# Kernel optimization log

Measured on AMD Instinct MI355X. Metric: run time of the kernel, lower is better.

## Reference

```python
import jax, jax.numpy as jnp
import numpy as np

HS = 1024          # hidden_size
NH_ATTN = 16       # attention heads
NH_LACT = 4        # lact fast-weight heads
DIN = HS // NH_LACT  # 256
DH = DIN             # inter_multi = 1
CHUNK = 1024       # lact_chunk_size
EPS = 1e-5


def setup_inputs() -> dict:
    key = jax.random.key(0)
    ks = jax.random.split(key, 6)
    B, S = 1, 4096
    x = jax.random.normal(ks[0], (B, S, HS), jnp.float32)
    ln_w = jnp.ones((HS,), jnp.float32)
    ln_b = jnp.zeros((HS,), jnp.float32)
    in_proj_w = jax.random.normal(ks[1], (3 * HS, HS), jnp.float32) * (HS ** -0.5)
    in_proj_b = jnp.zeros((3 * HS,), jnp.float32)
    out_proj_w = jax.random.normal(ks[2], (HS, HS), jnp.float32) * (HS ** -0.5)
    out_proj_b = jnp.zeros((HS,), jnp.float32)
    w0 = jax.random.normal(ks[3], (NH_LACT, DH, DIN), jnp.float32) / np.sqrt(DIN)
    w1 = jax.random.normal(ks[4], (NH_LACT, DIN, DH), jnp.float32) / np.sqrt(DH)
    w2 = jax.random.normal(ks[5], (NH_LACT, DH, DIN), jnp.float32) / np.sqrt(DIN)
    return dict(x=x, ln_w=ln_w, ln_b=ln_b, in_proj_w=in_proj_w, in_proj_b=in_proj_b,
                out_proj_w=out_proj_w, out_proj_b=out_proj_b, w0=w0, w1=w1, w2=w2)


def reference(x, ln_w, ln_b, in_proj_w, in_proj_b, out_proj_w, out_proj_b, w0, w1, w2):
    B, S, D = x.shape
    # LayerNorm
    mu = jnp.mean(x, axis=-1, keepdims=True)
    var = jnp.var(x, axis=-1, keepdims=True)
    xn = (x - mu) * jax.lax.rsqrt(var + EPS) * ln_w + ln_b

    # --- torch nn.MultiheadAttention(batch_first=True), self-attention, no mask ---
    qkv = xn @ in_proj_w.T + in_proj_b                      # [B,S,3D]
    q, k, v = jnp.split(qkv, 3, axis=-1)
    hd = D // NH_ATTN
    def heads(t):
        return t.reshape(B, S, NH_ATTN, hd).transpose(0, 2, 1, 3)  # [B,H,S,hd]
    q = heads(q) * (hd ** -0.5)
    k = heads(k)
    v = heads(v)
    attn = jax.nn.softmax(jnp.einsum('bhqd,bhkd->bhqk', q, k), axis=-1)
    ao = jnp.einsum('bhqk,bhkd->bhqd', attn, v).transpose(0, 2, 1, 3).reshape(B, S, D)
    attn_out = ao @ out_proj_w.T + out_proj_b

    # --- chunked fast-weight SwiGLU TTT (block_causal_lact_swiglu) ---
    # q=k=v=chunk; lr0=lr1=lr2=1; each outer chunk is one TTT step starting from
    # the module parameters: update weights on (k,v) then apply to q (block-causal).
    nc = S // CHUNK
    c = xn.reshape(B, nc, CHUNK, NH_LACT, DIN).transpose(0, 1, 3, 2, 4)  # [B,nc,nh,C,din]
    kv = c  # k == v == q == chunk

    # fast-weight SwiGLU forward on keys: f(k) = w1 @ (silu(w0 k) * (w2 k))
    gate = jnp.einsum('bnhcd,hed->bnhce', kv, w0)     # [B,nc,nh,C,dh]
    sg = jax.nn.sigmoid(gate)
    h = gate * sg                                     # silu
    g = jnp.einsum('bnhcd,hed->bnhce', kv, w2)
    hidden = h * g

    # negative dot-product loss L = -sum(v * f(k)) -> dOut = -v
    dout = -kv                                        # [B,nc,nh,C,din]
    dhid = jnp.einsum('bnhcd,hde->bnhce', dout, w1)
    dh = dhid * g
    dg = dhid * h
    dpre = dh * (sg + gate * sg * (1.0 - sg))         # silu'
    dw1 = jnp.einsum('bnhcd,bnhce->bnhde', dout, hidden)
    dw0 = jnp.einsum('bnhce,bnhcd->bnhed', dpre, kv)
    dw2 = jnp.einsum('bnhce,bnhcd->bnhed', dg, kv)

    # SGD step (lr = 1)
    w0n = w0 - dw0   # [B,nc,nh,dh,din]
    w1n = w1 - dw1
    w2n = w2 - dw2

    # apply updated fast weights to queries
    gq = jnp.einsum('bnhcd,bnhed->bnhce', c, w0n)
    hq = gq * jax.nn.sigmoid(gq)
    gq2 = jnp.einsum('bnhcd,bnhed->bnhce', c, w2n)
    oq = jnp.einsum('bnhce,bnhde->bnhcd', hq * gq2, w1n)  # [B,nc,nh,C,din]
    lact_out = oq.transpose(0, 1, 3, 2, 4).reshape(B, S, D)

    return lact_out + attn_out
```

## Files before the change

kernel.cpp:

```cpp
#include <hip/hip_runtime.h>
#include <hip/hip_bf16.h>


typedef __bf16 bf16_t;
typedef __bf16 bf16x8 __attribute__((ext_vector_type(8)));
typedef __bf16 bf16x4 __attribute__((ext_vector_type(4)));
typedef float  f32x4  __attribute__((ext_vector_type(4)));
typedef float  f32x16 __attribute__((ext_vector_type(16)));

#define SW64(r,cg) ((cg) ^ ((r)&7))
#define SW32(r,cg) ((cg) ^ (((r)>>2)&3))

static __device__ __forceinline__ f32x4 mfma16(bf16x8 a, bf16x8 b, f32x4 c){
  return __builtin_amdgcn_mfma_f32_16x16x32_bf16(a, b, c, 0, 0, 0);
}
static __device__ __forceinline__ f32x16 mfma32(bf16x8 a, bf16x8 b, f32x16 c){
  return __builtin_amdgcn_mfma_f32_32x32x16_bf16(a, b, c, 0, 0, 0);
}
__device__ __forceinline__ float sigm(float x){ return 1.0f/(1.0f + __expf(-x)); }
static __device__ __forceinline__ unsigned pkbf(float lo, float hi){
  unsigned short a = __builtin_bit_cast(unsigned short, (__bf16)lo);
  unsigned short b = __builtin_bit_cast(unsigned short, (__bf16)hi);
  return (unsigned)a | ((unsigned)b<<16);
}
static __device__ __forceinline__ float unpk_lo(unsigned u){
  return (float)__builtin_bit_cast(__bf16,(unsigned short)(u&0xffffu));
}
static __device__ __forceinline__ float unpk_hi(unsigned u){
  return (float)__builtin_bit_cast(__bf16,(unsigned short)(u>>16));
}
static __device__ __forceinline__ float hswap_add(float x){
  float a=x, b=x;
  asm volatile("v_permlane32_swap_b32 %0, %1" : "+v"(a), "+v"(b));
  return a+b;
}

__global__ __launch_bounds__(256) void ln_kernel(const float* __restrict__ x,
    const float* __restrict__ w, const float* __restrict__ b,
    bf16_t* __restrict__ xnb)
{
  int s = blockIdx.x, t = threadIdx.x;
  const float4* xr = (const float4*)(x + (size_t)s*1024);
  float4 v = xr[t];
  float sum = v.x+v.y+v.z+v.w;
  float ss  = v.x*v.x+v.y*v.y+v.z*v.z+v.w*v.w;
  #pragma unroll
  for (int o=32;o>0;o>>=1){ sum += __shfl_down(sum,o); ss += __shfl_down(ss,o); }
  __shared__ float red[8];
  __shared__ float stats[2];
  int wid=t>>6, lane=t&63;
  if(lane==0){ red[wid]=sum; red[4+wid]=ss; }
  __syncthreads();
  if(t==0){
    float S0=red[0]+red[1]+red[2]+red[3];
    float Q0=red[4]+red[5]+red[6]+red[7];
    float mu=S0*(1.0f/1024.0f);
    float var=Q0*(1.0f/1024.0f)-mu*mu;
    stats[0]=mu; stats[1]=rsqrtf(var+1e-5f);
  }
  __syncthreads();
  float mu=stats[0], rs=stats[1];
  float4 wv=((const float4*)w)[t], bv=((const float4*)b)[t];
  float4 o;
  o.x=(v.x-mu)*rs*wv.x+bv.x;
  o.y=(v.y-mu)*rs*wv.y+bv.y;
  o.z=(v.z-mu)*rs*wv.z+bv.z;
  o.w=(v.w-mu)*rs*wv.w+bv.w;
  bf16x4 ob = { (bf16_t)o.x, (bf16_t)o.y, (bf16_t)o.z, (bf16_t)o.w };
  *(bf16x4*)&xnb[(size_t)s*1024 + t*4] = ob;
}

__global__ __launch_bounds__(256) void prep_weights(
  const float* __restrict__ ipw, const float* __restrict__ opw,
  const float* __restrict__ w0, const float* __restrict__ w2,
  const float* __restrict__ w1,
  bf16_t* __restrict__ ipwb, bf16_t* __restrict__ opwb,
  bf16_t* __restrict__ w0b, bf16_t* __restrict__ w2b, bf16_t* __restrict__ w1tb)
{
  long i = ((long)blockIdx.x*256 + threadIdx.x)*4;
  if (i < 3145728) {
    float4 v = *(const float4*)(ipw + i);
    bf16x4 o = {(bf16_t)v.x,(bf16_t)v.y,(bf16_t)v.z,(bf16_t)v.w};
    *(bf16x4*)&ipwb[i] = o;
  } else if (i < 4194304) {
    long j = i - 3145728;
    float4 v = *(const float4*)(opw + j);
    bf16x4 o = {(bf16_t)v.x,(bf16_t)v.y,(bf16_t)v.z,(bf16_t)v.w};
    *(bf16x4*)&opwb[j] = o;
  } else if (i < 4456448) {
    long j = i - 4194304;
    float4 v = *(const float4*)(w0 + j);
    bf16x4 o = {(bf16_t)v.x,(bf16_t)v.y,(bf16_t)v.z,(bf16_t)v.w};
    *(bf16x4*)&w0b[j] = o;
  } else if (i < 4718592) {
    long j = i - 4456448;
    float4 v = *(const float4*)(w2 + j);
    bf16x4 o = {(bf16_t)v.x,(bf16_t)v.y,(bf16_t)v.z,(bf16_t)v.w};
    *(bf16x4*)&w2b[j] = o;
  } else if (i < 4980736) {
    long j = i - 4718592;
    int h = (int)(j>>16), rem = (int)(j&65535), d = rem>>8, e0 = rem&255;
    float4 v = *(const float4*)(w1 + j);
    bf16_t* dst = w1tb + h*65536 + d;
    dst[(e0+0)*256] = (bf16_t)v.x;
    dst[(e0+1)*256] = (bf16_t)v.y;
    dst[(e0+2)*256] = (bf16_t)v.z;
    dst[(e0+3)*256] = (bf16_t)v.w;
  }
}

__global__ __launch_bounds__(256) void xnT_kernel(const bf16_t* __restrict__ xnb,
                                                  bf16_t* __restrict__ xt)
{
  int dt = blockIdx.x, ct = blockIdx.y, bz = blockIdx.z;
  int nb = bz>>2, hb = bz&3;
  int t = threadIdx.x;
  __shared__ __align__(16) bf16_t T[4096];
  int r = t>>2, seg = t&3;
  const bf16_t* src = xnb + ((size_t)nb*1024 + ct*64 + r)*1024 + hb*256 + dt*64 + seg*16;
  uint4 a0 = *(const uint4*)src;
  uint4 a1 = *(const uint4*)(src + 8);
  *(uint4*)&T[r*64 + ((((seg*2  )&7)^(r&7))<<3)] = a0;
  *(uint4*)&T[r*64 + ((((seg*2+1)&7)^(r&7))<<3)] = a1;
  __syncthreads();
  int d = t>>2, s2 = t&3;
  unsigned uu[8];
  #pragma unroll
  for (int p=0;p<8;p++){
    int c0 = s2*16 + 2*p, c1 = c0+1;
    unsigned short e0 = __builtin_bit_cast(unsigned short,
        T[c0*64 + (((d>>3)^(c0&7))<<3) + (d&7)]);
    unsigned short e1 = __builtin_bit_cast(unsigned short,
        T[c1*64 + (((d>>3)^(c1&7))<<3) + (d&7)]);
    uu[p] = (unsigned)e0 | ((unsigned)e1<<16);
  }
  uint4 o0 = {uu[0],uu[1],uu[2],uu[3]}, o1 = {uu[4],uu[5],uu[6],uu[7]};
  bf16_t* dst = xt + (size_t)bz*262144 + (size_t)(dt*64 + d)*1024 + ct*64 + s2*16;
  *(uint4*)dst = o0;
  *(uint4*)(dst+8) = o1;
}

__device__ __forceinline__ void gemm_core(
    const bf16_t* __restrict__ A, int lda,
    const bf16_t* __restrict__ B, int ldb,
    int K, int m0, int n0, f32x4 (&acc)[4][4])
{
  int t = threadIdx.x, l = t&63;
  int w = t>>6, wr = w>>1, wc = w&1;
  __shared__ __align__(16) bf16_t As[4096], Bs[4096];
  int r0 = t>>2, c0 = t&3, r1 = r0+64;
  const bf16_t* Arow0 = A + (size_t)(m0+r0)*lda + c0*8;
  const bf16_t* Arow1 = A + (size_t)(m0+r1)*lda + c0*8;
  const bf16_t* Brow0 = B + (size_t)(n0+r0)*ldb + c0*8;
  const bf16_t* Brow1 = B + (size_t)(n0+r1)*ldb + c0*8;
  uint4 av0 = *(const uint4*)Arow0, av1 = *(const uint4*)Arow1;
  uint4 bv0 = *(const uint4*)Brow0, bv1 = *(const uint4*)Brow1;
  int wo0 = r0*32 + (SW32(r0,c0)<<3), wo1 = r1*32 + (SW32(r1,c0)<<3);

  for (int k0=0; k0<K; k0+=32) {
    if (k0) __syncthreads();
    *(uint4*)&As[wo0] = av0; *(uint4*)&As[wo1] = av1;
    *(uint4*)&Bs[wo0] = bv0; *(uint4*)&Bs[wo1] = bv1;
    __syncthreads();
    if (k0+32 < K) {
      av0 = *(const uint4*)(Arow0 + k0+32); av1 = *(const uint4*)(Arow1 + k0+32);
      bv0 = *(const uint4*)(Brow0 + k0+32); bv1 = *(const uint4*)(Brow1 + k0+32);
    }
    bf16x8 af[4], bb[4];
    #pragma unroll
    for (int mt=0;mt<4;mt++){
      int row = (wr<<6)+(mt<<4)+(l&15);
      af[mt] = *(bf16x8*)&As[row*32 + (SW32(row, (l>>4))<<3)];
    }
    #pragma unroll
    for (int nt=0;nt<4;nt++){
      int row = (wc<<6)+(nt<<4)+(l&15);
      bb[nt] = *(bf16x8*)&Bs[row*32 + (SW32(row, (l>>4))<<3)];
    }
    #pragma unroll
    for (int mt=0;mt<4;mt++)
      #pragma unroll
      for (int nt=0;nt<4;nt++)
        acc[mt][nt] = mfma16(af[mt], bb[nt], acc[mt][nt]);
  }
}

__device__ __forceinline__ void gemm_core_w(
    const bf16_t* __restrict__ A, int lda,
    const bf16_t* __restrict__ B, int ldb,
    int K, int m0, int n0, f32x4 (&acc)[4][2])
{
  int t = threadIdx.x, l = t&63;
  int w = t>>6, wr = w>>1, wc = w&1;
  __shared__ __align__(16) bf16_t As[4096], Bs[2048];
  int r0 = t>>2, c0 = t&3, r1 = r0+64;
  const bf16_t* Arow0 = A + (size_t)(m0+r0)*lda + c0*8;
  const bf16_t* Arow1 = A + (size_t)(m0+r1)*lda + c0*8;
  const bf16_t* Brow  = B + (size_t)(n0+r0)*ldb + c0*8;
  uint4 av0 = *(const uint4*)Arow0, av1 = *(const uint4*)Arow1;
  uint4 bv  = *(const uint4*)Brow;
  int wo0 = r0*32 + (SW32(r0,c0)<<3), wo1 = r1*32 + (SW32(r1,c0)<<3);

  for (int k0=0; k0<K; k0+=32) {
    if (k0) __syncthreads();
    *(uint4*)&As[wo0] = av0; *(uint4*)&As[wo1] = av1;
    *(uint4*)&Bs[wo0] = bv;
    __syncthreads();
    if (k0+32 < K) {
      av0 = *(const uint4*)(Arow0 + k0+32); av1 = *(const uint4*)(Arow1 + k0+32);
      bv  = *(const uint4*)(Brow + k0+32);
    }
    bf16x8 af[4], bb[2];
    #pragma unroll
    for (int mt=0;mt<4;mt++){
      int row = (wr<<6)+(mt<<4)+(l&15);
      af[mt] = *(bf16x8*)&As[row*32 + (SW32(row, (l>>4))<<3)];
    }
    #pragma unroll
    for (int nt=0;nt<2;nt++){
      int row = (wc<<5)+(nt<<4)+(l&15);
      bb[nt] = *(bf16x8*)&Bs[row*32 + (SW32(row, (l>>4))<<3)];
    }
    #pragma unroll
    for (int mt=0;mt<4;mt++)
      #pragma unroll
      for (int nt=0;nt<2;nt++)
        acc[mt][nt] = mfma16(af[mt], bb[nt], acc[mt][nt]);
  }
}

#define EPILOOP(...) { int l=threadIdx.x&63, w_=threadIdx.x>>6, wr=w_>>1, wc=w_&1; \
  _Pragma("unroll") for(int mt=0;mt<4;mt++) _Pragma("unroll") for(int nt=0;nt<4;nt++) \
  _Pragma("unroll") for(int q=0;q<4;q++){ \
    int gr=m0+(wr<<6)+(mt<<4)+((l>>4)<<2)+q; int gc=n0+(wc<<6)+(nt<<4)+(l&15); \
    float v=acc[mt][nt][q]; __VA_ARGS__ } }

#define ACCZERO(acc) \
  _Pragma("unroll") for(int i_=0;i_<4;i_++) _Pragma("unroll") for(int j_=0;j_<4;j_++){ \
    f32x4 z_={0.f,0.f,0.f,0.f}; acc[i_][j_]=z_; }

#define ACCZERO_W(acc) \
  _Pragma("unroll") for(int i_=0;i_<4;i_++) _Pragma("unroll") for(int j_=0;j_<2;j_++){ \
    f32x4 z_={0.f,0.f,0.f,0.f}; acc[i_][j_]=z_; }

template<int EPI>
__global__ __launch_bounds__(256) void gemm_big(
  const bf16_t* __restrict__ A, const bf16_t* __restrict__ B,
  float* __restrict__ C, const float* __restrict__ bias,
  bf16_t* __restrict__ O1, bf16_t* __restrict__ O2, bf16_t* __restrict__ O3,
  int K, int ldc)
{
  int m0 = blockIdx.y<<7, n0 = blockIdx.x<<7;
  f32x4 acc[4][4];
  ACCZERO(acc)
  gemm_core(A, K, B, K, K, m0, n0, acc);
  EPILOOP(
    if constexpr (EPI==1) {
      C[(size_t)gr*ldc + gc] = v + bias[gc];
    } else {
      v += bias[gc];
      int seg = gc>>10; int c2 = gc&1023; int hh = c2>>6; int dd = c2&63;
      size_t oi = ((size_t)hh*4096 + gr)*64 + dd;
      if (seg==0)      O1[oi] = (bf16_t)(v*0.18033688011112042f);
      else if (seg==1) O2[oi] = (bf16_t)v;
      else             O3[oi] = (bf16_t)v;
    }
  )
}

__global__ __launch_bounds__(256) void lact_fwd_ew(
    const bf16_t* __restrict__ xnb,
    const bf16_t* __restrict__ w0b, const bf16_t* __restrict__ w2b,
    const bf16_t* __restrict__ w1tb,
    bf16_t* __restrict__ hT, bf16_t* __restrict__ pT, bf16_t* __restrict__ gT)
{
  int bz = blockIdx.z, hb = bz&3;
  const bf16_t* A = xnb + (size_t)(bz>>2)*1048576 + (size_t)hb*256;
  int m0 = blockIdx.y<<7, n0 = blockIdx.x<<6;
  f32x4 acc[4][2];
  unsigned gpk[4][2][2], ppk[4][2][2];

  ACCZERO_W(acc)
  gemm_core_w(A, 1024, w0b + hb*65536, 256, 256, m0, n0, acc);
  #pragma unroll
  for (int mt=0;mt<4;mt++)
    #pragma unroll
    for (int nt=0;nt<2;nt++){
      gpk[mt][nt][0] = pkbf(acc[mt][nt][0], acc[mt][nt][1]);
      gpk[mt][nt][1] = pkbf(acc[mt][nt][2], acc[mt][nt][3]);
    }
  __syncthreads();
  ACCZERO_W(acc)
  gemm_core_w(A, 1024, w2b + hb*65536, 256, 256, m0, n0, acc);
  #pragma unroll
  for (int mt=0;mt<4;mt++)
    #pragma unroll
    for (int nt=0;nt<2;nt++){
      ppk[mt][nt][0] = pkbf(acc[mt][nt][0], acc[mt][nt][1]);
      ppk[mt][nt][1] = pkbf(acc[mt][nt][2], acc[mt][nt][3]);
    }
  __syncthreads();
  ACCZERO_W(acc)
  gemm_core_w(A, 1024, w1tb + hb*65536, 256, 256, m0, n0, acc);

  int l=threadIdx.x&63, w_=threadIdx.x>>6, wr=w_>>1, wc=w_&1;
  size_t tb = (size_t)bz*262144;
  #pragma unroll
  for (int mt=0;mt<4;mt++){
    #pragma unroll
    for (int nt=0;nt<2;nt++){
      int gc = n0 + (wc<<5) + (nt<<4) + (l&15);
      size_t rowoff = tb + (size_t)gc*1024;
      #pragma unroll
      for (int qp=0;qp<2;qp++){
        int gr0 = m0 + (wr<<6) + (mt<<4) + ((l>>4)<<2) + 2*qp;
        float gate0 = unpk_lo(gpk[mt][nt][qp]), gate1 = unpk_hi(gpk[mt][nt][qp]);
        float g0 = unpk_lo(ppk[mt][nt][qp]), g1 = unpk_hi(ppk[mt][nt][qp]);
        float dh0 = acc[mt][nt][2*qp], dh1 = acc[mt][nt][2*qp+1];
        float sg0 = sigm(gate0), sg1 = sigm(gate1);
        float hs0 = gate0*sg0, hs1 = gate1*sg1;
        float hid0 = hs0*g0, hid1 = hs1*g1;
        float nd0 = -dh0, nd1 = -dh1;
        float dpre0 = nd0*g0*(sg0 + gate0*sg0*(1.0f-sg0));
        float dpre1 = nd1*g1*(sg1 + gate1*sg1*(1.0f-sg1));
        float dg0 = nd0*hs0, dg1 = nd1*hs1;
        *(unsigned*)&hT[rowoff + gr0] = pkbf(hid0, hid1);
        *(unsigned*)&pT[rowoff + gr0] = pkbf(dpre0, dpre1);
        *(unsigned*)&gT[rowoff + gr0] = pkbf(dg0, dg1);
      }
    }
  }
}

__global__ __launch_bounds__(256) void lact_apply_u(
    const bf16_t* __restrict__ xnb,
    const bf16_t* __restrict__ w0nb, const bf16_t* __restrict__ w2nb,
    bf16_t* __restrict__ u)
{
  int bz = blockIdx.z;
  const bf16_t* A = xnb + (size_t)(bz>>2)*1048576 + (size_t)(bz&3)*256;
  int m0 = blockIdx.y<<7, n0 = blockIdx.x<<6;
  f32x4 acc[4][2];
  unsigned qpk[4][2][2];

  ACCZERO_W(acc)
  gemm_core_w(A, 1024, w2nb + (size_t)bz*65536, 256, 256, m0, n0, acc);
  #pragma unroll
  for (int mt=0;mt<4;mt++)
    #pragma unroll
    for (int nt=0;nt<2;nt++){
      qpk[mt][nt][0] = pkbf(acc[mt][nt][0], acc[mt][nt][1]);
      qpk[mt][nt][1] = pkbf(acc[mt][nt][2], acc[mt][nt][3]);
    }
  __syncthreads();
  ACCZERO_W(acc)
  gemm_core_w(A, 1024, w0nb + (size_t)bz*65536, 256, 256, m0, n0, acc);

  int l=threadIdx.x&63, w_=threadIdx.x>>6, wr=w_>>1, wc=w_&1;
  size_t tb = (size_t)bz*262144;
  #pragma unroll
  for (int mt=0;mt<4;mt++){
    #pragma unroll
    for (int nt=0;nt<2;nt++){
      int gc = n0 + (wc<<5) + (nt<<4) + (l&15);
      #pragma unroll
      for (int qp=0;qp<2;qp++){
        int gr0 = m0 + (wr<<6) + (mt<<4) + ((l>>4)<<2) + 2*qp;
        float q20 = unpk_lo(qpk[mt][nt][qp]), q21 = unpk_hi(qpk[mt][nt][qp]);
        float gq0 = acc[mt][nt][2*qp], gq1 = acc[mt][nt][2*qp+1];
        u[tb + (size_t)gr0*256 + gc]     = (bf16_t)(gq0*sigm(gq0)*q20);
        u[tb + (size_t)(gr0+1)*256 + gc] = (bf16_t)(gq1*sigm(gq1)*q21);
      }
    }
  }
}

__global__ __launch_bounds__(256) void lact_upd(
    const bf16_t* __restrict__ xnTb, const bf16_t* __restrict__ hTb,
    const bf16_t* __restrict__ pTb,  const bf16_t* __restrict__ gTb,
    const float* __restrict__ w1, const float* __restrict__ w0,
    const float* __restrict__ w2,
    bf16_t* __restrict__ w1nb, bf16_t* __restrict__ w0nb, bf16_t* __restrict__ w2nb)
{
  int zz = blockIdx.z, sub = zz>>4, bz = zz&15, hb = bz&3;
  const bf16_t* A = (sub==0? xnTb : (sub==1? pTb : gTb)) + (size_t)bz*262144;
  const bf16_t* B = (sub==0? hTb : xnTb) + (size_t)bz*262144;
  const float*  P = (sub==0? w1 : (sub==1? w0 : w2)) + (size_t)hb*65536;
  bf16_t*       O = (sub==0? w1nb : (sub==1? w0nb : w2nb)) + (size_t)bz*65536;
  float sgn = (sub==0) ? 1.0f : -1.0f;
  int m0 = blockIdx.y<<7, n0 = blockIdx.x<<6;
  f32x4 acc[4][2];
  ACCZERO_W(acc)
  gemm_core_w(A, 1024, B, 1024, 1024, m0, n0, acc);
  int l=threadIdx.x&63, w_=threadIdx.x>>6, wr=w_>>1, wc=w_&1;
  #pragma unroll
  for (int mt=0;mt<4;mt++){
    #pragma unroll
    for (int nt=0;nt<2;nt++){
      int gc = n0 + (wc<<5) + (nt<<4) + (l&15);
      #pragma unroll
      for (int q=0;q<4;q++){
        int gr = m0 + (wr<<6) + (mt<<4) + ((l>>4)<<2) + q;
        O[(size_t)gr*256 + gc] =
            (bf16_t)(P[(size_t)gr*256 + gc] + sgn*acc[mt][nt][q]);
      }
    }
  }
}

__global__ __launch_bounds__(256) void lact_final(
    const bf16_t* __restrict__ u, const bf16_t* __restrict__ w1nb,
    float* __restrict__ out)
{
  int bz = blockIdx.z;
  const bf16_t* A = u + (size_t)bz*262144;
  const bf16_t* B = w1nb + (size_t)bz*65536;
  float* C = out + (size_t)(bz>>2)*1048576 + (size_t)(bz&3)*256;
  int m0 = blockIdx.y<<7, n0 = (blockIdx.x&1)<<7;
  f32x4 acc[4][4];
  ACCZERO(acc)
  gemm_core(A, 256, B, 256, 256, m0, n0, acc);
  EPILOOP( C[(size_t)gr*1024 + gc] += v; )
}

__global__ __launch_bounds__(256) void vtrans(const bf16_t* __restrict__ Vb,
                                              bf16_t* __restrict__ Vt)
{
  int st = blockIdx.x, h = blockIdx.y, t = threadIdx.x;
  __shared__ __align__(16) bf16_t T[64*72];
  #pragma unroll
  for (int G=t; G<512; G+=256) {
    int r = G>>3, cg = G&7;
    *(uint4*)&T[r*72 + cg*8] =
      *(const uint4*)(Vb + ((size_t)h*4096 + st*64 + r)*64 + cg*8);
  }
  __syncthreads();
  int d = t>>2, seg = t&3;
  bf16x8 e0, e1;
  #pragma unroll
  for (int i=0;i<8;i++)  e0[i] = T[(seg*16+i)*72 + d];
  #pragma unroll
  for (int i=0;i<8;i++)  e1[i] = T[(seg*16+8+i)*72 + d];
  size_t base = ((size_t)h*64 + d)*4096 + st*64 + seg*16;
  *(bf16x8*)(Vt + base)     = e0;
  *(bf16x8*)(Vt + base + 8) = e1;
}

__global__ __launch_bounds__(256) void attn_mfma3(
    const bf16_t* __restrict__ Qb, const bf16_t* __restrict__ Kb,
    const bf16_t* __restrict__ Vt, float* __restrict__ Opart,
    float* __restrict__ lpart)
{
  int h = blockIdx.x, qblk = blockIdx.y, z = blockIdx.z;
  int t = threadIdx.x, w = t>>6, l = t&63;
  int lh = l>>5, lq = l&31;
  __shared__ __align__(16) bf16_t Ks[4096], Vs[4096];

  const bf16_t* Kg = Kb + (size_t)h*262144 + (size_t)z*131072;
  const bf16_t* Vg = Vt + (size_t)h*262144 + (size_t)z*2048;

  bf16x8 qf[4];
  {
    const bf16_t* Qg = Qb + ((size_t)h*4096 + (size_t)qblk*128 + w*32 + lq)*64 + lh*8;
    #pragma unroll
    for (int s=0;s<4;s++) qf[s] = *(const bf16x8*)(Qg + s*16);
  }

  int r0 = t>>3, c0 = t&7, r1 = r0+32;
  uint4 kv0 = *(const uint4*)(Kg + (size_t)r0*64 + c0*8);
  uint4 kv1 = *(const uint4*)(Kg + (size_t)r1*64 + c0*8);
  uint4 vv0 = *(const uint4*)(Vg + (size_t)r0*4096 + c0*8);
  uint4 vv1 = *(const uint4*)(Vg + (size_t)r1*4096 + c0*8);

  float l_r = 0.f;
  f32x16 Oa, Ob;
  #pragma unroll
  for (int i=0;i<16;i++){ Oa[i]=0.f; Ob[i]=0.f; }

  int wo0 = r0*64 + (SW64(r0,c0)<<3);
  int wo1 = r1*64 + (SW64(r1,c0)<<3);

  for (int kt=0; kt<32; ++kt) {
    __syncthreads();
    *(uint4*)&Ks[wo0] = kv0;
    *(uint4*)&Ks[wo1] = kv1;
    *(uint4*)&Vs[wo0] = vv0;
    *(uint4*)&Vs[wo1] = vv1;
    __syncthreads();
    if (kt < 31) {
      const bf16_t* Kg2 = Kg + (size_t)(kt+1)*4096;
      kv0 = *(const uint4*)(Kg2 + (size_t)r0*64 + c0*8);
      kv1 = *(const uint4*)(Kg2 + (size_t)r1*64 + c0*8);
      const bf16_t* Vg2 = Vg + (kt+1)*64;
      vv0 = *(const uint4*)(Vg2 + (size_t)r0*4096 + c0*8);
      vv1 = *(const uint4*)(Vg2 + (size_t)r1*4096 + c0*8);
    }
    f32x16 S0, S1;
    #pragma unroll
    for (int i=0;i<16;i++){ S0[i]=0.f; S1[i]=0.f; }
    __builtin_amdgcn_s_setprio(1);
    #pragma unroll
    for (int s=0;s<4;s++){
      int g = (s<<1) + lh;
      bf16x8 k0 = *(const bf16x8*)&Ks[lq*64 + (SW64(lq,g)<<3)];
      int rowb = 32 + lq;
      bf16x8 k1 = *(const bf16x8*)&Ks[rowb*64 + (SW64(rowb,g)<<3)];
      S0 = mfma32(k0, qf[s], S0);
      S1 = mfma32(k1, qf[s], S1);
    }
    __builtin_amdgcn_s_setprio(0);
    #pragma unroll
    for (int i=0;i<16;i++) S0[i] = exp2f(S0[i]);
    #pragma unroll
    for (int i=0;i<16;i++) S1[i] = exp2f(S1[i]);
    float rt[8];
    #pragma unroll
    for (int i=0;i<8;i++) rt[i] = (S0[i]+S0[i+8]) + (S1[i]+S1[i+8]);
    #pragma unroll
    for (int i=0;i<4;i++) rt[i] += rt[i+4];
    l_r += (rt[0]+rt[1])+(rt[2]+rt[3]);
    unsigned pk0[4][2], pk1[4][2];
    #pragma unroll
    for (int u2=0; u2<4; u2++){
      #pragma unroll
      for (int wd=0; wd<2; wd++){
        int q0 = 4*u2 + 2*wd;
        pk0[u2][wd] = pkbf(S0[q0], S0[q0+1]);
        pk1[u2][wd] = pkbf(S1[q0], S1[q0+1]);
      }
    }
    __builtin_amdgcn_s_setprio(1);
    #pragma unroll
    for (int ks=0; ks<4; ks++){
      int v0 = 2*(ks&1);
      unsigned x0, x1, y0, y1;
      if (ks < 2) { x0 = pk0[v0][0]; x1 = pk0[v0][1]; y0 = pk0[v0+1][0]; y1 = pk0[v0+1][1]; }
      else        { x0 = pk1[v0][0]; x1 = pk1[v0][1]; y0 = pk1[v0+1][0]; y1 = pk1[v0+1][1]; }
      asm volatile("v_permlane32_swap_b32 %0, %1" : "+v"(x0), "+v"(y0));
      asm volatile("v_permlane32_swap_b32 %0, %1" : "+v"(x1), "+v"(y1));
      uint4 pau = {x0, x1, y0, y1};
      bf16x8 pa = __builtin_bit_cast(bf16x8, pau);
      int g = (ks<<1) + lh;
      bf16x8 vf0 = *(const bf16x8*)&Vs[lq*64 + (SW64(lq,g)<<3)];
      int rowb = 32 + lq;
      bf16x8 vf1 = *(const bf16x8*)&Vs[rowb*64 + (SW64(rowb,g)<<3)];
      Oa = mfma32(pa, vf0, Oa);
      Ob = mfma32(pa, vf1, Ob);
    }
    __builtin_amdgcn_s_setprio(0);
  }
  l_r = hswap_add(l_r);
  size_t pb = ((size_t)(h*32+qblk))*2 + z;
  float* Op = Opart + pb*8192 + (size_t)(w*32)*64;
  #pragma unroll
  for (int reg=0; reg<16; reg++){
    int row = (reg&3) + 8*(reg>>2) + 4*lh;
    Op[row*64 + lq]      = Oa[reg];
    Op[row*64 + 32 + lq] = Ob[reg];
  }
  if (l < 32) {
    lpart[pb*128 + (size_t)(w*32+l)] = l_r;
  }
}

__global__ __launch_bounds__(256) void attn_merge(
    const float* __restrict__ Opart, const float* __restrict__ lpart,
    bf16_t* __restrict__ ao)
{
  int h = blockIdx.x, qblk = blockIdx.y, t = threadIdx.x;
  int r = t>>1, ch = (t&1)<<5;
  size_t b = ((size_t)(h*32+qblk))*2;
  const float* O0 = Opart + b*8192;
  const float* O1 = O0 + 8192;
  float inv = 1.0f/(lpart[b*128 + r] + lpart[b*128 + 128 + r]);
  bf16_t* dst = ao + (size_t)(qblk*128+r)*1024 + h*64 + ch;
  const float* p0 = O0 + r*64 + ch;
  const float* p1 = O1 + r*64 + ch;
  #pragma unroll
  for (int j=0;j<8;j++){
    float4 o0 = *(const float4*)(p0 + j*4);
    float4 o1 = *(const float4*)(p1 + j*4);
    bf16x4 ov;
    ov[0]=(bf16_t)((o0.x+o1.x)*inv);
    ov[1]=(bf16_t)((o0.y+o1.y)*inv);
    ov[2]=(bf16_t)((o0.z+o1.z)*inv);
    ov[3]=(bf16_t)((o0.w+o1.w)*inv);
    *(bf16x4*)(dst + j*4) = ov;
  }
}

extern "C" void kernel_launch(void* const* d_in, const int* in_sizes, int n_in,
                              void* d_out, int out_size, void* d_ws, size_t ws_size,
                              hipStream_t stream) {
  const float* x          = (const float*)d_in[0];
  const float* ln_w       = (const float*)d_in[1];
  const float* ln_b       = (const float*)d_in[2];
  const float* in_proj_w  = (const float*)d_in[3];
  const float* in_proj_b  = (const float*)d_in[4];
  const float* out_proj_w = (const float*)d_in[5];
  const float* out_proj_b = (const float*)d_in[6];
  const float* w0         = (const float*)d_in[7];
  const float* w1         = (const float*)d_in[8];
  const float* w2         = (const float*)d_in[9];
  float* out = (float*)d_out;

  float* ws = (float*)d_ws;
  bf16_t* xnb  = (bf16_t*)(ws);
  bf16_t* Qb   = (bf16_t*)(ws + 2097152);
  bf16_t* Kb   = (bf16_t*)(ws + 4194304);
  bf16_t* Vb   = (bf16_t*)(ws + 6291456);
  bf16_t* ub   = (bf16_t*)(ws + 6291456);
  bf16_t* aob  = (bf16_t*)(ws + 10485760);
  bf16_t* Vtp  = (bf16_t*)(ws + 14680064);
  bf16_t* xnTb = (bf16_t*)(ws + 18874368);
  bf16_t* hTb  = (bf16_t*)(ws + 20971520);
  bf16_t* pTb  = (bf16_t*)(ws + 23068672);
  bf16_t* gTb  = (bf16_t*)(ws + 25165824);
  float*  Opart= ws + 18874368;
  bf16_t* ipwb = (bf16_t*)(ws + 27262976);
  float*  lp   = ws + 27262976;
  bf16_t* opwb = (bf16_t*)(ws + 28835840);
  bf16_t* w0b  = (bf16_t*)(ws + 29360128);
  bf16_t* w2b  = (bf16_t*)(ws + 29491200);
  bf16_t* w1tb = (bf16_t*)(ws + 29622272);
  bf16_t* w0nb = (bf16_t*)(ws + 29753344);
  bf16_t* w1nb = (bf16_t*)(ws + 30277632);
  bf16_t* w2nb = (bf16_t*)(ws + 30801920);

  dim3 blk(256);

  ln_kernel<<<dim3(4096),blk,0,stream>>>(x, ln_w, ln_b, xnb);

  prep_weights<<<dim3(4864),blk,0,stream>>>(in_proj_w, out_proj_w, w0, w2, w1,
                                            ipwb, opwb, w0b, w2b, w1tb);

  gemm_big<3><<<dim3(24,32),blk,0,stream>>>(
      xnb, ipwb, nullptr, in_proj_b, Qb, Kb, Vb, 1024, 0);

  vtrans<<<dim3(64,16),blk,0,stream>>>(Vb, Vtp);

  attn_mfma3<<<dim3(16,32,2),blk,0,stream>>>(Qb, Kb, Vtp, Opart, lp);

  attn_merge<<<dim3(16,32),blk,0,stream>>>(Opart, lp, aob);

  gemm_big<1><<<dim3(8,32),blk,0,stream>>>(
      aob, opwb, out, out_proj_b, nullptr,nullptr,nullptr, 1024, 1024);

  xnT_kernel<<<dim3(4,16,16),blk,0,stream>>>(xnb, xnTb);

  lact_fwd_ew<<<dim3(4,8,16),blk,0,stream>>>(xnb, w0b, w2b, w1tb, hTb, pTb, gTb);

  lact_upd<<<dim3(4,2,48),blk,0,stream>>>(xnTb, hTb, pTb, gTb,
                                          w1, w0, w2, w1nb, w0nb, w2nb);

  lact_apply_u<<<dim3(4,8,16),blk,0,stream>>>(xnb, w0nb, w2nb, ub);

  lact_final<<<dim3(2,8,16),blk,0,stream>>>(ub, w1nb, out);
}
```

Measured before the change: 385.6 us.

## Double-buffer GEMM and attention tiles via direct global-to-LDS async loads

Replaces the register-staged global loads plus LDS stores in the GEMM cores and the attention kernel with global_load_lds direct copies into double-buffered shared memory, prefetching the next K-tile while the current one is consumed. Swizzling moves to the global address side so LDS writes stay linear. The attention inner loop is also split into two 32-row halves to reduce live S registers. The cost is doubled LDS footprint, which may lower occupancy, and one barrier per iteration is kept.

Result: slower. 395.9 us (+2.7%).

```diff
diff --git a/kernel.cpp b/kernel.cpp
--- a/kernel.cpp
+++ b/kernel.cpp
@@ -33,6 +33,11 @@
   float a=x, b=x;
   asm volatile("v_permlane32_swap_b32 %0, %1" : "+v"(a), "+v"(b));
   return a+b;
+}
+static __device__ __forceinline__ void gload16(const bf16_t* g, bf16_t* l){
+  __builtin_amdgcn_global_load_lds(
+      (const __attribute__((address_space(1))) void*)g,
+      (__attribute__((address_space(3))) void*)l, 16, 0, 0);
 }
 
 __global__ __launch_bounds__(256) void ln_kernel(const float* __restrict__ x,
@@ -147,41 +152,45 @@
 {
   int t = threadIdx.x, l = t&63;
   int w = t>>6, wr = w>>1, wc = w&1;
-  __shared__ __align__(16) bf16_t As[4096], Bs[4096];
-  int r0 = t>>2, c0 = t&3, r1 = r0+64;
-  const bf16_t* Arow0 = A + (size_t)(m0+r0)*lda + c0*8;
-  const bf16_t* Arow1 = A + (size_t)(m0+r1)*lda + c0*8;
-  const bf16_t* Brow0 = B + (size_t)(n0+r0)*ldb + c0*8;
-  const bf16_t* Brow1 = B + (size_t)(n0+r1)*ldb + c0*8;
-  uint4 av0 = *(const uint4*)Arow0, av1 = *(const uint4*)Arow1;
-  uint4 bv0 = *(const uint4*)Brow0, bv1 = *(const uint4*)Brow1;
-  int wo0 = r0*32 + (SW32(r0,c0)<<3), wo1 = r1*32 + (SW32(r1,c0)<<3);
-
+  __shared__ __align__(16) bf16_t As[2][4096], Bs[2][4096];
+  int row0 = t>>2, gs0 = t&3;
+  int swz = (gs0 ^ ((row0>>2)&3))<<3;
+  const bf16_t* Aa = A + (size_t)(m0+row0)*lda + swz;
+  const bf16_t* Ba = B + (size_t)(n0+row0)*ldb + swz;
+  size_t lda64 = (size_t)64*lda, ldb64 = (size_t)64*ldb;
+
+  gload16(Aa,         &As[0][t*8]);
+  gload16(Aa + lda64, &As[0][(t+256)*8]);
+  gload16(Ba,         &Bs[0][t*8]);
+  gload16(Ba + ldb64, &Bs[0][(t+256)*8]);
+  __syncthreads();
+  int cur = 0;
   for (int k0=0; k0<K; k0+=32) {
-    if (k0) __syncthreads();
-    *(uint4*)&As[wo0] = av0; *(uint4*)&As[wo1] = av1;
-    *(uint4*)&Bs[wo0] = bv0; *(uint4*)&Bs[wo1] = bv1;
-    __syncthreads();
     if (k0+32 < K) {
-      av0 = *(const uint4*)(Arow0 + k0+32); av1 = *(const uint4*)(Arow1 + k0+32);
-      bv0 = *(const uint4*)(Brow0 + k0+32); bv1 = *(const uint4*)(Brow1 + k0+32);
+      int nb2 = cur^1;
+      gload16(Aa + k0+32,         &As[nb2][t*8]);
+      gload16(Aa + lda64 + k0+32, &As[nb2][(t+256)*8]);
+      gload16(Ba + k0+32,         &Bs[nb2][t*8]);
+      gload16(Ba + ldb64 + k0+32, &Bs[nb2][(t+256)*8]);
     }
     bf16x8 af[4], bb[4];
     #pragma unroll
     for (int mt=0;mt<4;mt++){
       int row = (wr<<6)+(mt<<4)+(l&15);
-      af[mt] = *(bf16x8*)&As[row*32 + (SW32(row, (l>>4))<<3)];
+      af[mt] = *(bf16x8*)&As[cur][row*32 + (SW32(row, (l>>4))<<3)];
     }
     #pragma unroll
     for (int nt=0;nt<4;nt++){
       int row = (wc<<6)+(nt<<4)+(l&15);
-      bb[nt] = *(bf16x8*)&Bs[row*32 + (SW32(row, (l>>4))<<3)];
+      bb[nt] = *(bf16x8*)&Bs[cur][row*32 + (SW32(row, (l>>4))<<3)];
     }
     #pragma unroll
     for (int mt=0;mt<4;mt++)
       #pragma unroll
       for (int nt=0;nt<4;nt++)
         acc[mt][nt] = mfma16(af[mt], bb[nt], acc[mt][nt]);
+    __syncthreads();
+    cur ^= 1;
   }
 }
 
@@ -192,40 +201,43 @@
 {
   int t = threadIdx.x, l = t&63;
   int w = t>>6, wr = w>>1, wc = w&1;
-  __shared__ __align__(16) bf16_t As[4096], Bs[2048];
-  int r0 = t>>2, c0 = t&3, r1 = r0+64;
-  const bf16_t* Arow0 = A + (size_t)(m0+r0)*lda + c0*8;
-  const bf16_t* Arow1 = A + (size_t)(m0+r1)*lda + c0*8;
-  const bf16_t* Brow  = B + (size_t)(n0+r0)*ldb + c0*8;
-  uint4 av0 = *(const uint4*)Arow0, av1 = *(const uint4*)Arow1;
-  uint4 bv  = *(const uint4*)Brow;
-  int wo0 = r0*32 + (SW32(r0,c0)<<3), wo1 = r1*32 + (SW32(r1,c0)<<3);
-
+  __shared__ __align__(16) bf16_t As[2][4096], Bs[2][2048];
+  int row0 = t>>2, gs0 = t&3;
+  int swz = (gs0 ^ ((row0>>2)&3))<<3;
+  const bf16_t* Aa = A + (size_t)(m0+row0)*lda + swz;
+  const bf16_t* Ba = B + (size_t)(n0+row0)*ldb + swz;
+  size_t lda64 = (size_t)64*lda;
+
+  gload16(Aa,         &As[0][t*8]);
+  gload16(Aa + lda64, &As[0][(t+256)*8]);
+  gload16(Ba,         &Bs[0][t*8]);
+  __syncthreads();
+  int cur = 0;
   for (int k0=0; k0<K; k0+=32) {
-    if (k0) __syncthreads();
-    *(uint4*)&As[wo0] = av0; *(uint4*)&As[wo1] = av1;
-    *(uint4*)&Bs[wo0] = bv;
-    __syncthreads();
     if (k0+32 < K) {
-      av0 = *(const uint4*)(Arow0 + k0+32); av1 = *(const uint4*)(Arow1 + k0+32);
-      bv  = *(const uint4*)(Brow + k0+32);
+      int nb2 = cur^1;
+      gload16(Aa + k0+32,         &As[nb2][t*8]);
+      gload16(Aa + lda64 + k0+32, &As[nb2][(t+256)*8]);
+      gload16(Ba + k0+32,         &Bs[nb2][t*8]);
     }
     bf16x8 af[4], bb[2];
     #pragma unroll
     for (int mt=0;mt<4;mt++){
       int row = (wr<<6)+(mt<<4)+(l&15);
-      af[mt] = *(bf16x8*)&As[row*32 + (SW32(row, (l>>4))<<3)];
+      af[mt] = *(bf16x8*)&As[cur][row*32 + (SW32(row, (l>>4))<<3)];
     }
     #pragma unroll
     for (int nt=0;nt<2;nt++){
       int row = (wc<<5)+(nt<<4)+(l&15);
-      bb[nt] = *(bf16x8*)&Bs[row*32 + (SW32(row, (l>>4))<<3)];
+      bb[nt] = *(bf16x8*)&Bs[cur][row*32 + (SW32(row, (l>>4))<<3)];
     }
     #pragma unroll
     for (int mt=0;mt<4;mt++)
       #pragma unroll
       for (int nt=0;nt<2;nt++)
         acc[mt][nt] = mfma16(af[mt], bb[nt], acc[mt][nt]);
+    __syncthreads();
+    cur ^= 1;
   }
 }
 
@@ -289,7 +301,6 @@
       gpk[mt][nt][0] = pkbf(acc[mt][nt][0], acc[mt][nt][1]);
       gpk[mt][nt][1] = pkbf(acc[mt][nt][2], acc[mt][nt][3]);
     }
-  __syncthreads();
   ACCZERO_W(acc)
   gemm_core_w(A, 1024, w2b + hb*65536, 256, 256, m0, n0, acc);
   #pragma unroll
@@ -299,7 +310,6 @@
       ppk[mt][nt][0] = pkbf(acc[mt][nt][0], acc[mt][nt][1]);
       ppk[mt][nt][1] = pkbf(acc[mt][nt][2], acc[mt][nt][3]);
     }
-  __syncthreads();
   ACCZERO_W(acc)
   gemm_core_w(A, 1024, w1tb + hb*65536, 256, 256, m0, n0, acc);
 
@@ -352,7 +362,6 @@
       qpk[mt][nt][0] = pkbf(acc[mt][nt][0], acc[mt][nt][1]);
       qpk[mt][nt][1] = pkbf(acc[mt][nt][2], acc[mt][nt][3]);
     }
-  __syncthreads();
   ACCZERO_W(acc)
   gemm_core_w(A, 1024, w0nb + (size_t)bz*65536, 256, 256, m0, n0, acc);
 
@@ -446,7 +455,7 @@
   *(bf16x8*)(Vt + base + 8) = e1;
 }
 
-__global__ __launch_bounds__(256) void attn_mfma3(
+__global__ __launch_bounds__(256) void attn_mfma4(
     const bf16_t* __restrict__ Qb, const bf16_t* __restrict__ Kb,
     const bf16_t* __restrict__ Vt, float* __restrict__ Opart,
     float* __restrict__ lpart)
@@ -454,7 +463,7 @@
   int h = blockIdx.x, qblk = blockIdx.y, z = blockIdx.z;
   int t = threadIdx.x, w = t>>6, l = t&63;
   int lh = l>>5, lq = l&31;
-  __shared__ __align__(16) bf16_t Ks[4096], Vs[4096];
+  __shared__ __align__(16) bf16_t Ks[2][4096], Vs[2][4096];
 
   const bf16_t* Kg = Kb + (size_t)h*262144 + (size_t)z*131072;
   const bf16_t* Vg = Vt + (size_t)h*262144 + (size_t)z*2048;
@@ -466,89 +475,81 @@
     for (int s=0;s<4;s++) qf[s] = *(const bf16x8*)(Qg + s*16);
   }
 
-  int r0 = t>>3, c0 = t&7, r1 = r0+32;
-  uint4 kv0 = *(const uint4*)(Kg + (size_t)r0*64 + c0*8);
-  uint4 kv1 = *(const uint4*)(Kg + (size_t)r1*64 + c0*8);
-  uint4 vv0 = *(const uint4*)(Vg + (size_t)r0*4096 + c0*8);
-  uint4 vv1 = *(const uint4*)(Vg + (size_t)r1*4096 + c0*8);
+  int srow = t>>3, sgs = t&7;
+  const bf16_t* ka = Kg + (size_t)srow*64   + ((sgs^(srow&7))<<3);
+  const bf16_t* va = Vg + (size_t)srow*4096 + ((sgs^(srow&7))<<3);
 
   float l_r = 0.f;
   f32x16 Oa, Ob;
   #pragma unroll
   for (int i=0;i<16;i++){ Oa[i]=0.f; Ob[i]=0.f; }
 
-  int wo0 = r0*64 + (SW64(r0,c0)<<3);
-  int wo1 = r1*64 + (SW64(r1,c0)<<3);
+  #define STAGE_ATTN(buf, kt) { \
+    gload16(ka + (size_t)(kt)*4096,          &Ks[buf][t*8]); \
+    gload16(ka + (size_t)(kt)*4096 + 2048,   &Ks[buf][(t+256)*8]); \
+    gload16(va + (size_t)(kt)*64,            &Vs[buf][t*8]); \
+    gload16(va + (size_t)(kt)*64 + 131072,   &Vs[buf][(t+256)*8]); }
+
+  STAGE_ATTN(0, 0)
+  __syncthreads();
+  int cur = 0;
 
   for (int kt=0; kt<32; ++kt) {
-    __syncthreads();
-    *(uint4*)&Ks[wo0] = kv0;
-    *(uint4*)&Ks[wo1] = kv1;
-    *(uint4*)&Vs[wo0] = vv0;
-    *(uint4*)&Vs[wo1] = vv1;
-    __syncthreads();
-    if (kt < 31) {
-      const bf16_t* Kg2 = Kg + (size_t)(kt+1)*4096;
-      kv0 = *(const uint4*)(Kg2 + (size_t)r0*64 + c0*8);
-      kv1 = *(const uint4*)(Kg2 + (size_t)r1*64 + c0*8);
-      const bf16_t* Vg2 = Vg + (kt+1)*64;
-      vv0 = *(const uint4*)(Vg2 + (size_t)r0*4096 + c0*8);
-      vv1 = *(const uint4*)(Vg2 + (size_t)r1*4096 + c0*8);
-    }
-    f32x16 S0, S1;
-    #pragma unroll
-    for (int i=0;i<16;i++){ S0[i]=0.f; S1[i]=0.f; }
+    if (kt < 31) STAGE_ATTN(cur^1, kt+1)
+    unsigned pk[2][4][2];
+    #pragma unroll
+    for (int half=0; half<2; ++half){
+      f32x16 S;
+      #pragma unroll
+      for (int i=0;i<16;i++) S[i]=0.f;
+      int krow = (half<<5) + lq;
+      __builtin_amdgcn_s_setprio(1);
+      #pragma unroll
+      for (int s=0;s<4;s++){
+        int g = (s<<1) + lh;
+        bf16x8 kf = *(const bf16x8*)&Ks[cur][krow*64 + (SW64(lq,g)<<3)];
+        S = mfma32(kf, qf[s], S);
+      }
+      __builtin_amdgcn_s_setprio(0);
+      #pragma unroll
+      for (int i=0;i<16;i++) S[i] = exp2f(S[i]);
+      float rt[8];
+      #pragma unroll
+      for (int i=0;i<8;i++) rt[i] = S[i]+S[i+8];
+      #pragma unroll
+      for (int i=0;i<4;i++) rt[i] += rt[i+4];
+      l_r += (rt[0]+rt[1])+(rt[2]+rt[3]);
+      #pragma unroll
+      for (int u2=0; u2<4; u2++){
+        #pragma unroll
+        for (int wd=0; wd<2; wd++){
+          int q0 = 4*u2 + 2*wd;
+          pk[half][u2][wd] = pkbf(S[q0], S[q0+1]);
+        }
+      }
+    }
     __builtin_amdgcn_s_setprio(1);
     #pragma unroll
-    for (int s=0;s<4;s++){
-      int g = (s<<1) + lh;
-      bf16x8 k0 = *(const bf16x8*)&Ks[lq*64 + (SW64(lq,g)<<3)];
-      int rowb = 32 + lq;
-      bf16x8 k1 = *(const bf16x8*)&Ks[rowb*64 + (SW64(rowb,g)<<3)];
-      S0 = mfma32(k0, qf[s], S0);
-      S1 = mfma32(k1, qf[s], S1);
-    }
-    __builtin_amdgcn_s_setprio(0);
-    #pragma unroll
-    for (int i=0;i<16;i++) S0[i] = exp2f(S0[i]);
-    #pragma unroll
-    for (int i=0;i<16;i++) S1[i] = exp2f(S1[i]);
-    float rt[8];
-    #pragma unroll
-    for (int i=0;i<8;i++) rt[i] = (S0[i]+S0[i+8]) + (S1[i]+S1[i+8]);
-    #pragma unroll
-    for (int i=0;i<4;i++) rt[i] += rt[i+4];
-    l_r += (rt[0]+rt[1])+(rt[2]+rt[3]);
-    unsigned pk0[4][2], pk1[4][2];
-    #pragma unroll
-    for (int u2=0; u2<4; u2++){
-      #pragma unroll
-      for (int wd=0; wd<2; wd++){
-        int q0 = 4*u2 + 2*wd;
-        pk0[u2][wd] = pkbf(S0[q0], S0[q0+1]);
-        pk1[u2][wd] = pkbf(S1[q0], S1[q0+1]);
-      }
-    }
-    __builtin_amdgcn_s_setprio(1);
-    #pragma unroll
     for (int ks=0; ks<4; ks++){
-      int v0 = 2*(ks&1);
-      unsigned x0, x1, y0, y1;
-      if (ks < 2) { x0 = pk0[v0][0]; x1 = pk0[v0][1]; y0 = pk0[v0+1][0]; y1 = pk0[v0+1][1]; }
-      else        { x0 = pk1[v0][0]; x1 = pk1[v0][1]; y0 = pk1[v0+1][0]; y1 = pk1[v0+1][1]; }
+      int hsel = ks>>1, v0 = 2*(ks&1);
+      unsigned x0 = pk[hsel][v0][0],   x1 = pk[hsel][v0][1];
+      unsigned y0 = pk[hsel][v0+1][0], y1 = pk[hsel][v0+1][1];
       asm volatile("v_permlane32_swap_b32 %0, %1" : "+v"(x0), "+v"(y0));
       asm volatile("v_permlane32_swap_b32 %0, %1" : "+v"(x1), "+v"(y1));
       uint4 pau = {x0, x1, y0, y1};
       bf16x8 pa = __builtin_bit_cast(bf16x8, pau);
       int g = (ks<<1) + lh;
-      bf16x8 vf0 = *(const bf16x8*)&Vs[lq*64 + (SW64(lq,g)<<3)];
+      bf16x8 vf0 = *(const bf16x8*)&Vs[cur][lq*64 + (SW64(lq,g)<<3)];
       int rowb = 32 + lq;
-      bf16x8 vf1 = *(const bf16x8*)&Vs[rowb*64 + (SW64(rowb,g)<<3)];
+      bf16x8 vf1 = *(const bf16x8*)&Vs[cur][rowb*64 + (SW64(lq,g)<<3)];
       Oa = mfma32(pa, vf0, Oa);
       Ob = mfma32(pa, vf1, Ob);
     }
     __builtin_amdgcn_s_setprio(0);
-  }
+    __syncthreads();
+    cur ^= 1;
+  }
+  #undef STAGE_ATTN
   l_r = hswap_add(l_r);
   size_t pb = ((size_t)(h*32+qblk))*2 + z;
   float* Op = Opart + pb*8192 + (size_t)(w*32)*64;
@@ -639,7 +640,7 @@
 
   vtrans<<<dim3(64,16),blk,0,stream>>>(Vb, Vtp);
 
-  attn_mfma3<<<dim3(16,32,2),blk,0,stream>>>(Qb, Kb, Vtp, Opart, lp);
+  attn_mfma4<<<dim3(16,32,2),blk,0,stream>>>(Qb, Kb, Vtp, Opart, lp);
 
   attn_merge<<<dim3(16,32),blk,0,stream>>>(Opart, lp, aob);
 
```
